# Kernel tuning notes

Measured on AMD Instinct MI355X. Metric: run time of the kernel, lower is better.

Reference implementation:

```python
import jax, jax.numpy as jnp
import numpy as np

BINS = 16
EDGE_KS = 11
EDGE_SIGMA = 1.5
EPS = 1e-9


def _gauss1d(ks, sigma):
    x = jnp.arange(ks, dtype=jnp.float32) - (ks - 1) / 2.0
    g = jnp.exp(-(x * x) / (2.0 * sigma * sigma))
    return g / jnp.sum(g)


def _conv2d(x, k):
    # x: [B,Cin,H,W], k: [Cout,Cin,kh,kw], VALID padding
    return jax.lax.conv_general_dilated(x, k, (1, 1), 'VALID',
                                        dimension_numbers=('NCHW', 'OIHW', 'NCHW'))


def _gaussian_blur(x, ks, sigma):
    g = _gauss1d(ks, sigma)
    k = jnp.outer(g, g)[None, None]  # [1,1,ks,ks]
    p = ks // 2
    xp = jnp.pad(x, ((0, 0), (0, 0), (p, p), (p, p)), mode='reflect')
    return _conv2d(xp, k)


# 8 neighbor offsets ordered by angle 0,45,...,315 (kornia canny convention)
_OFFS = [(0, 1), (1, 1), (1, 0), (1, -1), (0, -1), (-1, -1), (-1, 0), (-1, 1)]


def _dir_kernels(center, nbr):
    ks = np.zeros((8, 1, 3, 3), np.float32)
    for i, (dy, dx) in enumerate(_OFFS):
        ks[i, 0, 1, 1] = center
        ks[i, 0, 1 + dy, 1 + dx] = nbr
    return jnp.asarray(ks)


NMS_K = _dir_kernels(1.0, -1.0)   # center minus directional neighbor
HYST_K = _dir_kernels(0.0, 1.0)   # directional neighbor value
SOBEL = jnp.asarray(np.stack([
    np.array([[-1, 0, 1], [-2, 0, 2], [-1, 0, 1]], np.float32),
    np.array([[-1, -2, -1], [0, 0, 0], [1, 2, 1]], np.float32)])[:, None])  # [2,1,3,3]


def _canny_edges(gray, low=0.1, high=0.2):
    blurred = _gaussian_blur(gray, 5, 1.0)
    gp = jnp.pad(blurred, ((0, 0), (0, 0), (1, 1), (1, 1)), mode='edge')
    grads = _conv2d(gp, SOBEL)                       # [B,2,H,W]
    gx, gy = grads[:, :1], grads[:, 1:]
    mag = jnp.sqrt(gx * gx + gy * gy + 1e-6)
    ang = jnp.round(jnp.rad2deg(jnp.arctan2(gy, gx)) / 45.0)
    pos_i = jnp.mod(ang, 8).astype(jnp.int32)        # [B,1,H,W]
    neg_i = jnp.mod(ang + 4, 8).astype(jnp.int32)
    mp = jnp.pad(mag, ((0, 0), (0, 0), (1, 1), (1, 1)))
    nms = _conv2d(mp, NMS_K)                         # [B,8,H,W]
    pos = jnp.take_along_axis(nms, pos_i, axis=1)
    neg = jnp.take_along_axis(nms, neg_i, axis=1)
    mag = mag * (jnp.minimum(pos, neg) > 0.0)
    edges = (mag > low).astype(jnp.float32) * 0.5 + (mag > high).astype(jnp.float32) * 0.5

    def body(c):
        e, _ = c
        weak = (e == 0.5).astype(jnp.float32)
        strong = (e == 1.0).astype(jnp.float32)
        nb = _conv2d(jnp.pad(e, ((0, 0), (0, 0), (1, 1), (1, 1))), HYST_K)
        hm = jnp.any(nb == 1.0, axis=1, keepdims=True).astype(jnp.float32) * weak + strong
        return (hm + (hm == 0.0) * weak * 0.5, e)

    def cond(c):
        e, old = c
        return jnp.any(e != old)

    edges, _ = jax.lax.while_loop(cond, body, (edges, -jnp.ones_like(edges)))
    return (edges == 1.0).astype(jnp.float32)


def _normalize_map(m):
    B = m.shape[0]
    f = m.reshape(B, -1)
    mn = f.min(axis=1).reshape(B, 1, 1, 1)
    mx = f.max(axis=1).reshape(B, 1, 1, 1)
    return (m - mn) / (mx - mn + EPS)


def _srd(x_norm, mean, std, alpha, beta):
    B, C, H, W = x_norm.shape
    x = jnp.clip(x_norm * std + mean, 0.0, 1.0)
    gray = 0.299 * x[:, :1] + 0.587 * x[:, 1:2] + 0.114 * x[:, 2:3]
    edges = _canny_edges(gray)
    edge_density = _gaussian_blur(edges, EDGE_KS, EDGE_SIGMA)
    # per-image color histogram sparsity, batched via offset indices
    qc = jnp.round(x * (BINS - 1)).astype(jnp.int32)
    combined = qc[:, 0] * BINS * BINS + qc[:, 1] * BINS + qc[:, 2]   # [B,H,W]
    nbins = BINS ** 3
    flat = combined.reshape(B, -1) + (jnp.arange(B, dtype=jnp.int32) * nbins)[:, None]
    counts = jnp.zeros(B * nbins, jnp.float32).at[flat.reshape(-1)].add(1.0)
    probs = counts / float(H * W)
    sparsity = -jnp.log(probs[flat] + EPS).reshape(B, 1, H, W)
    fused = alpha * _normalize_map(edge_density) + beta * _normalize_map(sparsity)
    return jax.nn.sigmoid(fused)


def setup_inputs():
    key = jax.random.key(0)
    x_norm = jax.random.normal(key, (16, 3, 512, 512), jnp.float32)
    mean = jnp.array([0.485, 0.456, 0.406], jnp.float32).reshape(1, 3, 1, 1)
    std = jnp.array([0.229, 0.224, 0.225], jnp.float32).reshape(1, 3, 1, 1)
    return {'x_norm': x_norm, 'mean': mean, 'std': std,
            'alpha': jnp.float32(1.0), 'beta': jnp.float32(1.0)}


def reference(x_norm, mean, std, alpha, beta):
    return _srd(x_norm, mean, std, alpha, beta)
```

## Files before the change

### kernel.cpp

```cpp
#include <hip/hip_runtime.h>
#include <stdint.h>

#define NB 16
#define HH 512
#define WW 512
#define HW (HH*WW)
#define NBINS 4096

typedef unsigned long long u64;

__device__ __forceinline__ float clip01(float v){ return fminf(fmaxf(v, 0.0f), 1.0f); }
__device__ __forceinline__ int refl(int i, int n){ if (i < 0) i = -i; if (i >= n) i = 2*n - 2 - i; return i; }
__device__ __forceinline__ int clampi(int i, int lo, int hi){ return i < lo ? lo : (i > hi ? hi : i); }

__global__ void __launch_bounds__(256) k_gray(const float* __restrict__ x,
                                              const float* __restrict__ mean,
                                              const float* __restrict__ stdv,
                                              float* __restrict__ gray,
                                              uint16_t* __restrict__ comb,
                                              uint4* __restrict__ hist4)
{
#pragma clang fp contract(off)
  int b = blockIdx.x, tid = threadIdx.x;
  if (b < 64) hist4[b*256 + tid] = make_uint4(0u,0u,0u,0u);
  int img  = b >> 6;
  int base = (b & 63) * 4096;
  float m0 = mean[0], m1 = mean[1], m2 = mean[2];
  float s0 = stdv[0], s1 = stdv[1], s2 = stdv[2];
  const float* xb = x + (size_t)img * 3 * HW;
  float*     gb   = gray + (size_t)img*HW;
  uint16_t*  cb   = comb + (size_t)img*HW;
  #pragma unroll
  for (int it = 0; it < 4; it++){
    int f4 = it*256 + tid;
    int p  = base + f4*4;
    float4 r = *(const float4*)(xb + p);
    float4 g = *(const float4*)(xb + HW + p);
    float4 bl= *(const float4*)(xb + 2*HW + p);
    float xr[4] = {r.x, r.y, r.z, r.w};
    float xg[4] = {g.x, g.y, g.z, g.w};
    float xbl[4] = {bl.x, bl.y, bl.z, bl.w};
    float gy[4]; uint16_t cc[4];
    #pragma unroll
    for (int j = 0; j < 4; j++){
      float cr = clip01(xr[j]*s0 + m0);
      float cg = clip01(xg[j]*s1 + m1);
      float cbv= clip01(xbl[j]*s2 + m2);
      gy[j] = 0.299f*cr + 0.587f*cg + 0.114f*cbv;
      int c = ((int)rintf(cr*15.0f))*256 + ((int)rintf(cg*15.0f))*16 + (int)rintf(cbv*15.0f);
      cc[j] = (uint16_t)c;
    }
    *(float4*)(gb + p) = make_float4(gy[0], gy[1], gy[2], gy[3]);
    ushort4 cv; cv.x = cc[0]; cv.y = cc[1]; cv.z = cc[2]; cv.w = cc[3];
    *(ushort4*)(cb + p) = cv;
  }
}

__global__ void __launch_bounds__(256) k_canny(const float* __restrict__ gray,
                                               u64* __restrict__ A, u64* __restrict__ Sb)
{
#pragma clang fp contract(off)
  __shared__ float ubuf[40*73];
  __shared__ float blr[36*69];
  __shared__ uint8_t sdir[32*64];
  int b = blockIdx.x;
  int img = b >> 7;
  int t = b & 127;
  int y0 = (t >> 3) << 5;
  int x0 = (t & 7) << 6;
  const float* gb = gray + (size_t)img*HW;
  int tid = threadIdx.x;
  float g5[5]; { float s=0.0f; for(int i=0;i<5;i++){ float tt=(float)i-2.0f; g5[i]=expf(-(tt*tt)/2.0f); s+=g5[i]; } for(int i=0;i<5;i++) g5[i]/=s; }
  for (int i = tid; i < 40*72; i += 256){
    int ly = i/72, lx = i - ly*72;
    int gy = refl(y0 - 4 + ly, HH);
    int gx = refl(x0 - 4 + lx, WW);
    ubuf[ly*73 + lx] = gb[gy*WW + gx];
  }
  __syncthreads();
  for (int task = tid; task < 272; task += 256){
    int lx = task % 68;
    int ly = (task / 68) * 9;
    float w[5][5];
    #pragma unroll
    for (int j = 0; j < 4; j++)
      #pragma unroll
      for (int k = 0; k < 5; k++)
        w[j][k] = ubuf[(ly+j)*73 + lx + k];
    #pragma unroll
    for (int s = 0; s < 9; s++){
      #pragma unroll
      for (int k = 0; k < 5; k++) w[4][k] = ubuf[(ly+s+4)*73 + lx + k];
      float acc = 0.0f;
      #pragma unroll
      for (int ky = 0; ky < 5; ky++)
        #pragma unroll
        for (int kx = 0; kx < 5; kx++)
          acc += (g5[ky]*g5[kx]) * w[ky][kx];
      blr[(ly+s)*69 + lx] = acc;
      #pragma unroll
      for (int j = 0; j < 4; j++)
        #pragma unroll
        for (int k = 0; k < 5; k++) w[j][k] = w[j+1][k];
    }
  }
  __syncthreads();
  for (int i = tid; i < 34*66; i += 256){
    int ly = i/66, lx = i - ly*66;
    int Y = y0 - 1 + ly, X = x0 - 1 + lx;
    float m = 0.0f;
    if (Y >= 0 && Y < HH && X >= 0 && X < WW){
      float v[3][3];
      for (int dy = 0; dy < 3; dy++){
        int Yl = clampi(Y + dy - 1, 0, HH-1) - (y0 - 2);
        for (int dx = 0; dx < 3; dx++){
          int Xl = clampi(X + dx - 1, 0, WW-1) - (x0 - 2);
          v[dy][dx] = blr[Yl*69 + Xl];
        }
      }
      float gx = (v[0][2] - v[0][0]) + 2.0f*(v[1][2] - v[1][0]) + (v[2][2] - v[2][0]);
      float gy = (v[2][0] + 2.0f*v[2][1] + v[2][2]) - (v[0][0] + 2.0f*v[0][1] + v[0][2]);
      m = sqrtf(gx*gx + gy*gy + 1e-6f);
      if (ly >= 1 && ly <= 32 && lx >= 1 && lx <= 64){
        float ax = fabsf(gx), ay = fabsf(gy);
        int d;
        if (ay <= 0.41421356237309503f*ax) d = (gx >= 0.0f) ? 0 : 4;
        else if (ay >= 2.4142135623730951f*ax) d = (gy > 0.0f) ? 2 : 6;
        else if (gx > 0.0f) d = (gy > 0.0f) ? 1 : 7;
        else d = (gy > 0.0f) ? 3 : 5;
        sdir[(ly-1)*64 + (lx-1)] = (uint8_t)d;
      }
    }
    ubuf[ly*67 + lx] = m;
  }
  __syncthreads();
  const int OY[8] = {0,1,1,1,0,-1,-1,-1};
  const int OX[8] = {1,1,0,-1,-1,-1,0,1};
  int lane = tid & 63, wv = tid >> 6;
  for (int j = 0; j < 8; j++){
    int y = j*4 + wv;
    int xx0 = lane;
    float m = ubuf[(y+1)*67 + (xx0+1)];
    int d  = sdir[y*64 + xx0];
    int d2 = (d + 4) & 7;
    float mp = 0.0f, mn = 0.0f;
    { int yy=y+OY[d],  xx=xx0+OX[d];  int gy=y0+yy, gx=x0+xx; if(gy>=0&&gy<HH&&gx>=0&&gx<WW) mp = ubuf[(yy+1)*67 + (xx+1)]; }
    { int yy=y+OY[d2], xx=xx0+OX[d2]; int gy=y0+yy, gx=x0+xx; if(gy>=0&&gy<HH&&gx>=0&&gx<WW) mn = ubuf[(yy+1)*67 + (xx+1)]; }
    bool keep = ((m - mp) > 0.0f) && ((m - mn) > 0.0f);
    float mf = keep ? m : 0.0f;
    bool strong = mf > 0.2f;
    bool weak   = (mf > 0.1f) && !strong;
    u64 wb = __ballot(weak);
    u64 sb = __ballot(strong);
    if (lane == 0){
      int gy = y0 + y;
      A [img*4096 + gy*8 + (x0>>6)] = wb;
      Sb[img*4096 + gy*8 + (x0>>6)] = sb;
    }
  }
}

__device__ __forceinline__ u64 ks_flood(u64 g, u64 P){
  u64 p1 = P, g1 = g;
  g1 |= p1 & (g1 << 1);  p1 &= (p1 << 1);
  g1 |= p1 & (g1 << 2);  p1 &= (p1 << 2);
  g1 |= p1 & (g1 << 4);  p1 &= (p1 << 4);
  g1 |= p1 & (g1 << 8);  p1 &= (p1 << 8);
  g1 |= p1 & (g1 << 16); p1 &= (p1 << 16);
  g1 |= p1 & (g1 << 32);
  u64 p2 = P, g2 = g;
  g2 |= p2 & (g2 >> 1);  p2 &= (p2 >> 1);
  g2 |= p2 & (g2 >> 2);  p2 &= (p2 >> 2);
  g2 |= p2 & (g2 >> 4);  p2 &= (p2 >> 4);
  g2 |= p2 & (g2 >> 8);  p2 &= (p2 >> 8);
  g2 |= p2 & (g2 >> 16); p2 &= (p2 >> 16);
  g2 |= p2 & (g2 >> 32);
  return g1 | g2;
}

#define HROW(m, l, r_) ((m) | ((m)<<1) | ((m)>>1) | ((l)>>63) | ((r_)<<63))

#define UPD2(i) do{ \
    if (Pr[i] & ~Sr[i]){ \
      u64 Sv = Sr[i]; \
      u64 mu = ((i) > 0) ? Sr[(i)-1] : MU; \
      u64 md = ((i) < 7) ? Sr[(i)+1] : MD; \
      u64 lu = ((i) > 0) ? L[(i)-1]  : LUv; \
      u64 ldn= ((i) < 7) ? L[(i)+1]  : LDv; \
      u64 ru = ((i) > 0) ? Rr[(i)-1] : RUv; \
      u64 rdn= ((i) < 7) ? Rr[(i)+1] : RDv; \
      u64 nb = HROW(mu,lu,ru) | HROW(Sv,L[i],Rr[i]) | HROW(md,ldn,rdn); \
      u64 gg = Sv | (Pr[i] & nb); \
      if (gg != Sv){ \
        u64 ns = ks_flood(gg, Pr[i]); \
        Sr[i] = ns; sS[(r0+(i))*9+w] = ns; changed = true; \
      } \
    } \
  } while(0)

__global__ void __launch_bounds__(512) k_mid(const u64* __restrict__ A, u64* __restrict__ S,
                                             const uint16_t* __restrict__ comb,
                                             uint32_t* __restrict__ hist)
{
  __shared__ __align__(16) char smem[512*9*8];
  int tid = threadIdx.x;
  if (blockIdx.x < 16){
    u64* sS = (u64*)smem;
    int img = blockIdx.x;
    const u64* gA = A + img * 4096;
    u64*       gS = S + img * 4096;
    for (int i = tid; i < 4096; i += 512)
      sS[(i>>3)*9 + (i&7)] = gS[i];
    __syncthreads();
    int  w    = tid & 7;
    int  g    = tid >> 3;
    int  r0   = g << 3;
    bool left = (w > 0), right = (w < 7);
    bool topw = ((g & 7) != 0), botw = ((g & 7) != 7);
    bool topi = (r0 > 0),       boti = (r0 < 504);
    u64 Sr[8], Pr[8];
    #pragma unroll
    for (int i = 0; i < 8; i++){
      Sr[i] = sS[(r0+i)*9 + w];
      Pr[i] = gA[(r0+i)*8 + w] | Sr[i];
    }
    for (;;){
      bool changed = false;
      #pragma unroll 1
      for (int rep = 0; rep < 2; rep++){
        u64 L[8], Rr[8];
        #pragma unroll
        for (int i = 0; i < 8; i++){
          u64 lv = __shfl_up(Sr[i], 1);
          u64 rv = __shfl_down(Sr[i], 1);
          L[i]  = left  ? lv : 0ull;
          Rr[i] = right ? rv : 0ull;
        }
        u64 t7  = __shfl_up(Sr[7], 8);
        u64 t7l = __shfl_up(Sr[7], 9);
        u64 t7r = __shfl_up(Sr[7], 7);
        u64 b0  = __shfl_down(Sr[0], 8);
        u64 b0l = __shfl_down(Sr[0], 7);
        u64 b0r = __shfl_down(Sr[0], 9);
        u64 MU, LUv, RUv, MD, LDv, RDv;
        if (topw){      MU = t7; LUv = left ? t7l : 0ull; RUv = right ? t7r : 0ull; }
        else if (topi){ MU = sS[(r0-1)*9+w];
                        LUv = left  ? sS[(r0-1)*9+w-1] : 0ull;
                        RUv = right ? sS[(r0-1)*9+w+1] : 0ull; }
        else { MU = 0ull; LUv = 0ull; RUv = 0ull; }
        if (botw){      MD = b0; LDv = left ? b0l : 0ull; RDv = right ? b0r : 0ull; }
        else if (boti){ MD = sS[(r0+8)*9+w];
                        LDv = left  ? sS[(r0+8)*9+w-1] : 0ull;
                        RDv = right ? sS[(r0+8)*9+w+1] : 0ull; }
        else { MD = 0ull; LDv = 0ull; RDv = 0ull; }
        #pragma unroll
        for (int i = 0; i < 8; i++) UPD2(i);
        #pragma unroll
        for (int i = 7; i >= 0; i--) UPD2(i);
      }
      if (!__syncthreads_or(changed ? 1 : 0)) break;
    }
    #pragma unroll
    for (int i = 0; i < 8; i++) gS[(r0+i)*8 + w] = Sr[i];
  } else {
    uint32_t* h = (uint32_t*)smem;
    int pb  = blockIdx.x - 16;
    int img = pb >> 5;
    int base = (pb & 31) * 8192;
    for (int i = tid; i < NBINS; i += 512) h[i] = 0u;
    __syncthreads();
    const uint16_t* cb = comb + (size_t)img*HW;
    #pragma unroll
    for (int it = 0; it < 4; it++){
      int f4 = it*512 + tid;
      ushort4 cv = *(const ushort4*)(cb + base + f4*4);
      atomicAdd(&h[cv.x], 1u);
      atomicAdd(&h[cv.y], 1u);
      atomicAdd(&h[cv.z], 1u);
      atomicAdd(&h[cv.w], 1u);
    }
    __syncthreads();
    uint32_t* gh = hist + img * NBINS;
    for (int i = tid; i < NBINS; i += 512){ uint32_t v = h[i]; if (v) atomicAdd(&gh[i], v); }
  }
}

__global__ void __launch_bounds__(256) k_b11(const u64* __restrict__ S, float* __restrict__ out,
                                             float2* __restrict__ part)
{
#pragma clang fp contract(off)
  __shared__ u64 wds[74][3];
  __shared__ float hb[74][64];
  __shared__ float smn[4], smx[4];
  int b = blockIdx.x;
  int img = b >> 6;
  int t = b & 63;
  int y0 = (t >> 3) << 6;
  int tx = t & 7;
  int x0 = tx << 6;
  int tid = threadIdx.x;
  float g[11]; { float s=0.0f; for(int i=0;i<11;i++){ float tt=(float)i-5.0f; g[i]=expf(-(tt*tt)/4.5f); s+=g[i]; } for(int i=0;i<11;i++) g[i]/=s; }
  for (int i = tid; i < 74*3; i += 256){
    int j = i/3, widx = i - j*3;
    int gy = refl(y0 - 5 + j, HH);
    int gw = tx - 1 + widx;
    wds[j][widx] = (gw >= 0 && gw < 8) ? S[img*4096 + gy*8 + gw] : 0ull;
  }
  __syncthreads();
  for (int i = tid; i < 74*64; i += 256){
    int j = i >> 6, c = i & 63;
    float acc = 0.0f;
    for (int k = 0; k < 11; k++){
      int xx = refl(x0 + c + k - 5, WW);
      int widx = (xx >> 6) - tx + 1;
      float bv = (float)((wds[j][widx] >> (xx & 63)) & 1ull);
      acc += g[k] * bv;
    }
    hb[j][c] = acc;
  }
  __syncthreads();
  float mn = 3.4e38f, mx = -3.4e38f;
  float* ob = out + (size_t)img*HW;
  for (int i = tid; i < 4096; i += 256){
    int y = i >> 6, c = i & 63;
    float acc = 0.0f;
    for (int k = 0; k < 11; k++) acc += g[k] * hb[y + k][c];
    ob[(y0 + y)*WW + x0 + c] = acc;
    mn = fminf(mn, acc); mx = fmaxf(mx, acc);
  }
  for (int off = 32; off >= 1; off >>= 1){
    mn = fminf(mn, __shfl_down(mn, off));
    mx = fmaxf(mx, __shfl_down(mx, off));
  }
  int wv = tid >> 6, ln = tid & 63;
  if (ln == 0){ smn[wv] = mn; smx[wv] = mx; }
  __syncthreads();
  if (tid == 0){
    part[b] = make_float2(fminf(fminf(smn[0],smn[1]),fminf(smn[2],smn[3])),
                          fmaxf(fmaxf(smx[0],smx[1]),fmaxf(smx[2],smx[3])));
  }
}

__global__ void __launch_bounds__(256) k_edred(const float2* __restrict__ part,
                                               const uint32_t* __restrict__ hist,
                                               uint32_t* __restrict__ stats){
  __shared__ uint32_t sx[4], sn[4];
  int img = blockIdx.x;
  int tid = threadIdx.x;
  uint32_t mx = 0u, mn = 0xFFFFFFFFu;
  for (int i = tid; i < NBINS; i += 256){
    uint32_t c = hist[img*NBINS + i];
    if (c > mx) mx = c;
    if (c > 0u && c < mn) mn = c;
  }
  for (int off = 32; off >= 1; off >>= 1){
    uint32_t ox = (uint32_t)__shfl_down((int)mx, off);
    uint32_t on = (uint32_t)__shfl_down((int)mn, off);
    if (ox > mx) mx = ox;
    if (on < mn) mn = on;
  }
  int wv = tid >> 6, ln = tid & 63;
  if (ln == 0){ sx[wv] = mx; sn[wv] = mn; }
  float fmn = 3.4e38f, fmx = -3.4e38f;
  if (wv == 0){
    float2 v = part[img*64 + ln];
    fmn = v.x; fmx = v.y;
    for (int off = 32; off >= 1; off >>= 1){
      fmn = fminf(fmn, __shfl_down(fmn, off));
      fmx = fmaxf(fmx, __shfl_down(fmx, off));
    }
  }
  __syncthreads();
  if (tid == 0){
    uint32_t MX = max(max(sx[0],sx[1]), max(sx[2],sx[3]));
    uint32_t MN = min(min(sn[0],sn[1]), min(sn[2],sn[3]));
    stats[img*4+0] = __float_as_uint(fmn);
    stats[img*4+1] = __float_as_uint(fmx);
    stats[img*4+2] = __float_as_uint(-logf((float)MX / 262144.0f + 1e-9f));
    stats[img*4+3] = __float_as_uint(-logf((float)MN / 262144.0f + 1e-9f));
  }
}

__global__ void k_final(const float* __restrict__ ed, const uint16_t* __restrict__ comb,
                        const uint32_t* __restrict__ hist, const uint32_t* __restrict__ stats,
                        const float* __restrict__ alpha, const float* __restrict__ beta,
                        float* __restrict__ out)
{
#pragma clang fp contract(off)
  int idx = blockIdx.x * 256 + threadIdx.x;
  int img = idx >> 18;
  float a = alpha[0], b = beta[0];
  float mne = __uint_as_float(stats[img*4+0]);
  float mxe = __uint_as_float(stats[img*4+1]);
  float mns = __uint_as_float(stats[img*4+2]);
  float mxs = __uint_as_float(stats[img*4+3]);
  float e  = ed[idx];
  float sp = -logf((float)hist[img*NBINS + comb[idx]] / 262144.0f + 1e-9f);
  float en = (e  - mne) / (mxe - mne + 1e-9f);
  float sn = (sp - mns) / (mxs - mns + 1e-9f);
  float f  = a*en + b*sn;
  out[idx] = 1.0f / (1.0f + expf(-f));
}

extern "C" void kernel_launch(void* const* d_in, const int* in_sizes, int n_in,
                              void* d_out, int out_size, void* d_ws, size_t ws_size,
                              hipStream_t stream)
{
  const float* x     = (const float*)d_in[0];
  const float* mean  = (const float*)d_in[1];
  const float* stdv  = (const float*)d_in[2];
  const float* alpha = (const float*)d_in[3];
  const float* beta  = (const float*)d_in[4];
  float* out = (float*)d_out;

  char* ws = (char*)d_ws;
  float*    gray  = (float*)ws;
  uint16_t* comb  = (uint16_t*)(ws + (16u << 20));
  float2*   part  = (float2*)(ws + (24u << 20));
  uint32_t* hist  = (uint32_t*)(ws + (25u << 20));
  u64*      Ab    = (u64*)(ws + (26u << 20));
  u64*      Sb    = (u64*)(ws + (27u << 20));
  uint32_t* stats = (uint32_t*)(ws + (28u << 20));

  hipLaunchKernelGGL(k_gray,  dim3(1024),  dim3(256), 0, stream, x, mean, stdv, gray, comb, (uint4*)hist);
  hipLaunchKernelGGL(k_canny, dim3(2048),  dim3(256), 0, stream, gray, Ab, Sb);
  hipLaunchKernelGGL(k_mid,   dim3(528),   dim3(512), 0, stream, Ab, Sb, comb, hist);
  hipLaunchKernelGGL(k_b11,   dim3(1024),  dim3(256), 0, stream, Sb, out, part);
  hipLaunchKernelGGL(k_edred, dim3(NB),    dim3(256), 0, stream, part, hist, stats);
  hipLaunchKernelGGL(k_final, dim3(16384), dim3(256), 0, stream, out, comb, hist, stats, alpha, beta, out);
}
```

Measured before the change: 120.0 us.

## Skip idle wavefronts in hysteresis loop, vectorize final kernel, alias canny shared buffer

The hysteresis flood-fill in k_mid now tracks per-wavefront change flags in shared memory, using double buffering. A wavefront only recomputes when it or an adjacent wavefront changed in the previous round, which saves work once the fill has converged locally. k_final now processes four pixels per thread with float4 and ushort4 loads and launches a quarter as many blocks. k_canny places its direction buffer inside the unused tail of ubuf to cut LDS use per block. These changes add an extra barrier per iteration and rely on the aliased region being dead when sdir is written.

```diff
diff --git a/kernel.cpp b/kernel.cpp
--- a/kernel.cpp
+++ b/kernel.cpp
@@ -62,7 +62,7 @@
 #pragma clang fp contract(off)
   __shared__ float ubuf[40*73];
   __shared__ float blr[36*69];
-  __shared__ uint8_t sdir[32*64];
+  uint8_t* sdir = (uint8_t*)&ubuf[2278];
   int b = blockIdx.x;
   int img = b >> 7;
   int t = b & 127;
@@ -203,6 +203,7 @@
                                              uint32_t* __restrict__ hist)
 {
   __shared__ __align__(16) char smem[512*9*8];
+  __shared__ int wfl[2][12];
   int tid = threadIdx.x;
   if (blockIdx.x < 16){
     u64* sS = (u64*)smem;
@@ -211,10 +212,12 @@
     u64*       gS = S + img * 4096;
     for (int i = tid; i < 4096; i += 512)
       sS[(i>>3)*9 + (i&7)] = gS[i];
+    if (tid < 12){ wfl[0][tid] = (tid >= 1 && tid <= 8) ? 1 : 0; wfl[1][tid] = 0; }
     __syncthreads();
     int  w    = tid & 7;
     int  g    = tid >> 3;
     int  r0   = g << 3;
+    int  wvi  = tid >> 6;
     bool left = (w > 0), right = (w < 7);
     bool topw = ((g & 7) != 0), botw = ((g & 7) != 7);
     bool topi = (r0 > 0),       boti = (r0 < 504);
@@ -224,41 +227,49 @@
       Sr[i] = sS[(r0+i)*9 + w];
       Pr[i] = gA[(r0+i)*8 + w] | Sr[i];
     }
+    int pb = 0, cb = 1;
     for (;;){
+      bool act = (wfl[pb][wvi] | wfl[pb][wvi+1] | wfl[pb][wvi+2]) != 0;
       bool changed = false;
-      #pragma unroll 1
-      for (int rep = 0; rep < 2; rep++){
-        u64 L[8], Rr[8];
-        #pragma unroll
-        for (int i = 0; i < 8; i++){
-          u64 lv = __shfl_up(Sr[i], 1);
-          u64 rv = __shfl_down(Sr[i], 1);
-          L[i]  = left  ? lv : 0ull;
-          Rr[i] = right ? rv : 0ull;
+      if (act){
+        #pragma unroll 1
+        for (int rep = 0; rep < 2; rep++){
+          u64 L[8], Rr[8];
+          #pragma unroll
+          for (int i = 0; i < 8; i++){
+            u64 lv = __shfl_up(Sr[i], 1);
+            u64 rv = __shfl_down(Sr[i], 1);
+            L[i]  = left  ? lv : 0ull;
+            Rr[i] = right ? rv : 0ull;
+          }
+          u64 t7  = __shfl_up(Sr[7], 8);
+          u64 t7l = __shfl_up(Sr[7], 9);
+          u64 t7r = __shfl_up(Sr[7], 7);
+          u64 b0  = __shfl_down(Sr[0], 8);
+          u64 b0l = __shfl_down(Sr[0], 7);
+          u64 b0r = __shfl_down(Sr[0], 9);
+          u64 MU, LUv, RUv, MD, LDv, RDv;
+          if (topw){      MU = t7; LUv = left ? t7l : 0ull; RUv = right ? t7r : 0ull; }
+          else if (topi){ MU = sS[(r0-1)*9+w];
+                          LUv = left  ? sS[(r0-1)*9+w-1] : 0ull;
+                          RUv = right ? sS[(r0-1)*9+w+1] : 0ull; }
+          else { MU = 0ull; LUv = 0ull; RUv = 0ull; }
+          if (botw){      MD = b0; LDv = left ? b0l : 0ull; RDv = right ? b0r : 0ull; }
+          else if (boti){ MD = sS[(r0+8)*9+w];
+                          LDv = left  ? sS[(r0+8)*9+w-1] : 0ull;
+                          RDv = right ? sS[(r0+8)*9+w+1] : 0ull; }
+          else { MD = 0ull; LDv = 0ull; RDv = 0ull; }
+          #pragma unroll
+          for (int i = 0; i < 8; i++) UPD2(i);
+          #pragma unroll
+          for (int i = 7; i >= 0; i--) UPD2(i);
         }
-        u64 t7  = __shfl_up(Sr[7], 8);
-        u64 t7l = __shfl_up(Sr[7], 9);
-        u64 t7r = __shfl_up(Sr[7], 7);
-        u64 b0  = __shfl_down(Sr[0], 8);
-        u64 b0l = __shfl_down(Sr[0], 7);
-        u64 b0r = __shfl_down(Sr[0], 9);
-        u64 MU, LUv, RUv, MD, LDv, RDv;
-        if (topw){      MU = t7; LUv = left ? t7l : 0ull; RUv = right ? t7r : 0ull; }
-        else if (topi){ MU = sS[(r0-1)*9+w];
-                        LUv = left  ? sS[(r0-1)*9+w-1] : 0ull;
-                        RUv = right ? sS[(r0-1)*9+w+1] : 0ull; }
-        else { MU = 0ull; LUv = 0ull; RUv = 0ull; }
-        if (botw){      MD = b0; LDv = left ? b0l : 0ull; RDv = right ? b0r : 0ull; }
-        else if (boti){ MD = sS[(r0+8)*9+w];
-                        LDv = left  ? sS[(r0+8)*9+w-1] : 0ull;
-                        RDv = right ? sS[(r0+8)*9+w+1] : 0ull; }
-        else { MD = 0ull; LDv = 0ull; RDv = 0ull; }
-        #pragma unroll
-        for (int i = 0; i < 8; i++) UPD2(i);
-        #pragma unroll
-        for (int i = 7; i >= 0; i--) UPD2(i);
+        if (changed) wfl[cb][wvi+1] = 1;
       }
+      __syncthreads();
+      if (tid == (wvi << 6)) wfl[pb][wvi+1] = 0;
       if (!__syncthreads_or(changed ? 1 : 0)) break;
+      int ts = pb; pb = cb; cb = ts;
     }
     #pragma unroll
     for (int i = 0; i < 8; i++) gS[(r0+i)*8 + w] = Sr[i];
@@ -381,25 +392,35 @@
   }
 }
 
-__global__ void k_final(const float* __restrict__ ed, const uint16_t* __restrict__ comb,
+__global__ void __launch_bounds__(256) k_final(const float* __restrict__ ed,
+                        const uint16_t* __restrict__ comb,
                         const uint32_t* __restrict__ hist, const uint32_t* __restrict__ stats,
                         const float* __restrict__ alpha, const float* __restrict__ beta,
                         float* __restrict__ out)
 {
 #pragma clang fp contract(off)
   int idx = blockIdx.x * 256 + threadIdx.x;
-  int img = idx >> 18;
+  int img = idx >> 16;
   float a = alpha[0], b = beta[0];
   float mne = __uint_as_float(stats[img*4+0]);
   float mxe = __uint_as_float(stats[img*4+1]);
   float mns = __uint_as_float(stats[img*4+2]);
   float mxs = __uint_as_float(stats[img*4+3]);
-  float e  = ed[idx];
-  float sp = -logf((float)hist[img*NBINS + comb[idx]] / 262144.0f + 1e-9f);
-  float en = (e  - mne) / (mxe - mne + 1e-9f);
-  float sn = (sp - mns) / (mxs - mns + 1e-9f);
-  float f  = a*en + b*sn;
-  out[idx] = 1.0f / (1.0f + expf(-f));
+  float4 e4 = *(const float4*)(ed + (size_t)idx*4);
+  ushort4 c4 = *(const ushort4*)(comb + (size_t)idx*4);
+  const uint32_t* gh = hist + img*NBINS;
+  float ee[4] = {e4.x, e4.y, e4.z, e4.w};
+  uint16_t cc[4] = {c4.x, c4.y, c4.z, c4.w};
+  float oo[4];
+  #pragma unroll
+  for (int j = 0; j < 4; j++){
+    float sp = -logf((float)gh[cc[j]] / 262144.0f + 1e-9f);
+    float en = (ee[j] - mne) / (mxe - mne + 1e-9f);
+    float sn = (sp - mns) / (mxs - mns + 1e-9f);
+    float f  = a*en + b*sn;
+    oo[j] = 1.0f / (1.0f + expf(-f));
+  }
+  *(float4*)(out + (size_t)idx*4) = make_float4(oo[0], oo[1], oo[2], oo[3]);
 }
 
 extern "C" void kernel_launch(void* const* d_in, const int* in_sizes, int n_in,
@@ -427,5 +448,5 @@
   hipLaunchKernelGGL(k_mid,   dim3(528),   dim3(512), 0, stream, Ab, Sb, comb, hist);
   hipLaunchKernelGGL(k_b11,   dim3(1024),  dim3(256), 0, stream, Sb, out, part);
   hipLaunchKernelGGL(k_edred, dim3(NB),    dim3(256), 0, stream, part, hist, stats);
-  hipLaunchKernelGGL(k_final, dim3(16384), dim3(256), 0, stream, out, comb, hist, stats, alpha, beta, out);
-}
+  hipLaunchKernelGGL(k_final, dim3(4096),  dim3(256), 0, stream, out, comb, hist, stats, alpha, beta, out);
+}
```

Measured after the change: 117.8 us (median of 2 runs). No clear change (-1.8%).
